# Kernel optimization log

Measured on AMD Instinct MI355X. Metric: run time of the kernel, lower is better.

Reference implementation:

```python
import jax, jax.numpy as jnp
import numpy as np
from jax import lax

T, B = 80, 32
ACT, CIN, HID, LSTM_H = 16, 4, 512, 256

def _conv(x, w, b, stride, pad):
    y = lax.conv_general_dilated(x, w, (stride, stride), [(pad, pad), (pad, pad)],
                                 dimension_numbers=('NCHW', 'OIHW', 'NCHW'))
    return y + b[None, :, None, None]

def setup_inputs() -> dict:
    key = jax.random.key(0)
    ks = jax.random.split(key, 20)
    s = 0.02
    return {
        'x': jax.random.uniform(ks[0], (T, B, CIN, 84, 84), dtype=jnp.float32),
        'last_action': jax.random.randint(ks[1], (T, B), 0, ACT),
        'reward': jax.random.normal(ks[2], (T, B), dtype=jnp.float32),
        'dones': jnp.zeros((T, B), dtype=bool),
        'hx': jax.random.normal(ks[3], (2, B, LSTM_H), dtype=jnp.float32) * s,
        'conv1_w': jax.random.normal(ks[4], (32, CIN, 8, 8), jnp.float32) * s,
        'conv1_b': jnp.zeros((32,), jnp.float32),
        'conv2_w': jax.random.normal(ks[5], (64, 32, 4, 4), jnp.float32) * s,
        'conv2_b': jnp.zeros((64,), jnp.float32),
        'conv3_w': jax.random.normal(ks[6], (64, 64, 3, 3), jnp.float32) * s,
        'conv3_b': jnp.zeros((64,), jnp.float32),
        'fc_w': jax.random.normal(ks[7], (HID, 3136), jnp.float32) * s,
        'fc_b': jnp.zeros((HID,), jnp.float32),
        'lstm_wih': jax.random.normal(ks[8], (4 * LSTM_H, HID + ACT + 1), jnp.float32) * s,
        'lstm_whh': jax.random.normal(ks[9], (4 * LSTM_H, LSTM_H), jnp.float32) * s,
        'lstm_bih': jnp.zeros((4 * LSTM_H,), jnp.float32),
        'lstm_bhh': jnp.zeros((4 * LSTM_H,), jnp.float32),
        'actor_w': jax.random.normal(ks[10], (ACT, LSTM_H), jnp.float32) * s,
        'actor_b': jnp.zeros((ACT,), jnp.float32),
        'critic_w': jax.random.normal(ks[11], (1, LSTM_H), jnp.float32) * s,
        'critic_b': jnp.zeros((1,), jnp.float32),
    }

def reference(x, last_action, reward, dones, hx,
              conv1_w, conv1_b, conv2_w, conv2_b, conv3_w, conv3_b,
              fc_w, fc_b, lstm_wih, lstm_whh, lstm_bih, lstm_bhh,
              actor_w, actor_b, critic_w, critic_b):
    seq_len, bs = x.shape[0], x.shape[1]
    xf = x.reshape(seq_len * bs, CIN, 84, 84)          # combine time & batch
    la = jax.nn.one_hot(last_action.reshape(-1), ACT, dtype=jnp.float32)
    rw = reward.reshape(-1, 1)

    lrelu = lambda v: jax.nn.leaky_relu(v, 0.01)
    h = lrelu(_conv(xf, conv1_w, conv1_b, 4, 1))       # [N,32,20,20]
    h = lrelu(_conv(h, conv2_w, conv2_b, 2, 0))        # [N,64,9,9]
    h = lrelu(_conv(h, conv3_w, conv3_b, 1, 0))        # [N,64,7,7]
    h = h.reshape(h.shape[0], -1)                      # [N,3136]
    h = lrelu(h @ fc_w.T + fc_b)                       # [N,512]
    h = jnp.concatenate([h, rw, la], axis=1)           # [N,529]
    h = h.reshape(seq_len, bs, -1)

    def step(carry, inp):
        xt, dt = inp                                   # [bs,529], [bs] bool
        carry = jnp.where(dt[None, :, None], 0.0, carry)
        hh, cc = carry[0], carry[1]
        gates = xt @ lstm_wih.T + lstm_bih + hh @ lstm_whh.T + lstm_bhh
        i, f, g, o = jnp.split(gates, 4, axis=1)
        cc = jax.nn.sigmoid(f) * cc + jax.nn.sigmoid(i) * jnp.tanh(g)
        hh = jax.nn.sigmoid(o) * jnp.tanh(cc)
        return jnp.stack([hh, cc], 0), hh

    _, hs = lax.scan(step, hx, (h, dones))             # hs: [T,bs,256]
    feat = hs.reshape(seq_len * bs, LSTM_H)

    logits = feat @ actor_w.T + actor_b                # [N,16]
    values = feat @ critic_w.T + critic_b              # [N,1]
    logits = jnp.where(jnp.isnan(logits), jnp.float32(1e-12), logits)
    return logits.reshape(seq_len, -1, bs), values.reshape(seq_len, bs)
```

## Files before the change

kernel.cpp:

```cpp
#include <hip/hip_runtime.h>
#include <math.h>

#define T_ 80
#define B_ 32
#define N_ 2560
#define LH_ 256

typedef __attribute__((ext_vector_type(8))) short short8;
typedef __attribute__((ext_vector_type(4))) float f32x4;
#define MFMA16(a, b, c) __builtin_amdgcn_mfma_f32_16x16x32_bf16((a), (b), (c), 0, 0, 0)

__device__ __forceinline__ float lrelu(float v) { return v > 0.f ? v : 0.01f * v; }
__device__ __forceinline__ short f2bf(float f) {
    unsigned u = __float_as_uint(f);
    return (short)((u + 0x7fffu + ((u >> 16) & 1u)) >> 16);
}

__global__ void pack_all_k(const float* __restrict__ c1w, const float* __restrict__ c2w,
                           const float* __restrict__ c3w, const float* __restrict__ fcw,
                           const float* __restrict__ wih,
                           short* __restrict__ wp1, short* __restrict__ wp2,
                           short* __restrict__ wp3, short* __restrict__ wfcP,
                           short* __restrict__ wihP, int* __restrict__ cnt) {
    int blk = blockIdx.x, tidx = threadIdx.x;
    if (blk < 6272) {
        int g = blk * 256 + tidx;
        int j = g / 3136, kp = g % 3136, p = kp >> 6, oc = kp & 63;
        wfcP[g] = f2bf(fcw[j * 3136 + oc * 49 + p]);
        return;
    }
    blk -= 6272;
    if (blk < 2048) {
        int g = blk * 256 + tidx;
        int r = g >> 9, k = g & 511;
        wihP[g] = f2bf(wih[r * 529 + k]);
        return;
    }
    blk -= 2048;
    if (blk < 32) {
        int g = blk * 256 + tidx;
        int ky = g >> 10, oc = (g >> 5) & 31, k = g & 31, kx = k >> 2, ci = k & 3;
        wp1[g] = f2bf(c1w[((oc * 4 + ci) * 8 + ky) * 8 + kx]);
        return;
    }
    blk -= 32;
    if (blk < 128) {
        int g = blk * 256 + tidx;
        int t = g >> 11, oc = (g >> 5) & 63, ci = g & 31, ky = t >> 2, kx = t & 3;
        wp2[g] = f2bf(c2w[((oc * 32 + ci) * 4 + ky) * 4 + kx]);
        return;
    }
    blk -= 128;
    if (blk < 144) {
        int g = blk * 256 + tidx;
        int tkc = g >> 11, oc = (g >> 5) & 63, c32 = g & 31;
        int t = tkc >> 1, kc = tkc & 1, ky = t / 3, kx = t % 3;
        wp3[g] = f2bf(c3w[((oc * 64 + kc * 32 + c32) * 3 + ky) * 3 + kx]);
        return;
    }
    cnt[tidx] = 0; cnt[256 + tidx] = 0;
}

#define C1_RS 344
__global__ __launch_bounds__(512) void conv1_mfma(
    const float* __restrict__ x, const short* __restrict__ wp1,
    const float* __restrict__ bias, short* __restrict__ h1) {
    __shared__ short xs[44 * C1_RS];
    __shared__ short ob[208 * 32];
    int blk = blockIdx.x, n = blk >> 1, h = blk & 1, tid = threadIdx.x;
    for (int i = tid; i < 44 * 84; i += 512) {
        int ry = i / 84, xi4 = i % 84;
        int ci = xi4 / 21, x4 = xi4 % 21;
        int iy = ry + h * 40 - 1;
        if (iy < 0 || iy > 83) continue;
        float4 v = *(const float4*)(x + (size_t)(n * 4 + ci) * 7056 + iy * 84 + x4 * 4);
        int base = ry * C1_RS + (x4 * 4 + 1) * 4 + ci;
        xs[base] = f2bf(v.x); xs[base + 4] = f2bf(v.y);
        xs[base + 8] = f2bf(v.z); xs[base + 12] = f2bf(v.w);
    }
    for (int i = tid; i < 44 * 4; i += 512)
        xs[(i >> 2) * C1_RS + (i & 3)] = 0;
    if (h == 0) for (int i = tid; i < C1_RS; i += 512) xs[i] = 0;
    __syncthreads();

    int lane = tid & 63, wid = tid >> 6;
    int lr = lane & 15, kq = lane >> 4;
    short8 bfr[8][2];
#pragma unroll
    for (int ky = 0; ky < 8; ++ky)
#pragma unroll
        for (int nt = 0; nt < 2; ++nt)
            bfr[ky][nt] = *(const short8*)&wp1[((ky * 32) + nt * 16 + lr) * 32 + kq * 8];
    float b0 = bias[lr], b1 = bias[16 + lr];

    for (int t = wid; t < 13; t += 8) {
        int p = t * 16 + lr; if (p > 199) p = 199;
        int oy = p / 20, ox = p % 20;
        f32x4 acc0 = {0.f, 0.f, 0.f, 0.f}, acc1 = {0.f, 0.f, 0.f, 0.f};
#pragma unroll
        for (int ky = 0; ky < 8; ++ky) {
            int ry = oy * 4 + ky;
            short8 af = *(const short8*)&xs[ry * C1_RS + ox * 16 + kq * 8];
            acc0 = MFMA16(af, bfr[ky][0], acc0);
            acc1 = MFMA16(af, bfr[ky][1], acc1);
        }
        int pm = t * 16 + kq * 4;
#pragma unroll
        for (int r = 0; r < 4; ++r) {
            ob[(pm + r) * 32 + lr]      = f2bf(lrelu(acc0[r] + b0));
            ob[(pm + r) * 32 + 16 + lr] = f2bf(lrelu(acc1[r] + b1));
        }
    }
    __syncthreads();
    uint4* dst = (uint4*)(h1 + (size_t)n * 12800 + h * 6400);
    for (int i = tid; i < 800; i += 512) dst[i] = ((uint4*)ob)[i];
}

__global__ __launch_bounds__(512) void conv23_mfma(
    const short* __restrict__ h1,
    const short* __restrict__ wp2, const float* __restrict__ b2v,
    const short* __restrict__ wp3, const float* __restrict__ b3v,
    short* __restrict__ h3) {
    __shared__ short in_s[400 * 40];
    __shared__ short ob2[96 * 72];
    int n = blockIdx.x, tid = threadIdx.x;
    const uint4* src = (const uint4*)(h1 + (size_t)n * 12800);
    for (int i = tid; i < 1600; i += 512)
        *(uint4*)&in_s[(i >> 2) * 40 + (i & 3) * 8] = src[i];
    __syncthreads();
    int lane = tid & 63, wid = tid >> 6;
    int nt = wid & 3, mh = wid >> 2;
    int lr = lane & 15, kq = lane >> 4;
    {
        short8 bfr[16];
#pragma unroll
        for (int t = 0; t < 16; ++t)
            bfr[t] = *(const short8*)&wp2[(t * 64 + nt * 16 + lr) * 32 + kq * 8];
        float bl = b2v[nt * 16 + lr];
        for (int mt = mh * 3; mt < mh * 3 + 3; ++mt) {
            int p = mt * 16 + lr; if (p > 80) p = 80;
            int oy = p / 9, ox = p % 9;
            f32x4 acc = {0.f, 0.f, 0.f, 0.f};
#pragma unroll
            for (int ky = 0; ky < 4; ++ky)
#pragma unroll
                for (int kx = 0; kx < 4; ++kx) {
                    int pix = (oy * 2 + ky) * 20 + ox * 2 + kx;
                    short8 af = *(const short8*)&in_s[pix * 40 + kq * 8];
                    acc = MFMA16(af, bfr[ky * 4 + kx], acc);
                }
            int pm = mt * 16 + kq * 4;
#pragma unroll
            for (int r = 0; r < 4; ++r)
                ob2[(pm + r) * 72 + nt * 16 + lr] = f2bf(lrelu(acc[r] + bl));
        }
    }
    __syncthreads();
    {
        short8 cfr[18];
#pragma unroll
        for (int t = 0; t < 18; ++t)
            cfr[t] = *(const short8*)&wp3[(t * 64 + nt * 16 + lr) * 32 + kq * 8];
        float bl3 = b3v[nt * 16 + lr];
        short* ob3 = in_s;
        for (int mt = mh * 2; mt < mh * 2 + 2; ++mt) {
            int p = mt * 16 + lr; if (p > 48) p = 48;
            int oy = p / 7, ox = p % 7;
            f32x4 acc = {0.f, 0.f, 0.f, 0.f};
#pragma unroll
            for (int ky = 0; ky < 3; ++ky)
#pragma unroll
                for (int kx = 0; kx < 3; ++kx) {
                    int pix = (oy + ky) * 9 + ox + kx;
#pragma unroll
                    for (int kc = 0; kc < 2; ++kc) {
                        short8 af = *(const short8*)&ob2[pix * 72 + kc * 32 + kq * 8];
                        acc = MFMA16(af, cfr[(ky * 3 + kx) * 2 + kc], acc);
                    }
                }
            int pm = mt * 16 + kq * 4;
#pragma unroll
            for (int r = 0; r < 4; ++r)
                ob3[(pm + r) * 64 + nt * 16 + lr] = f2bf(lrelu(acc[r] + bl3));
        }
    }
    __syncthreads();
    uint4* dst = (uint4*)(h3 + (size_t)n * 3136);
    for (int i = tid; i < 392; i += 512) dst[i] = ((uint4*)in_s)[i];
}

template <int OUT>
__global__ __launch_bounds__(256) void gemm_bf16(
    const short* __restrict__ A, const short* __restrict__ B,
    const float* __restrict__ bias, void* __restrict__ Cout,
    int M, int N, int K, int ldc,
    const float* __restrict__ reward = nullptr, const int* __restrict__ la = nullptr,
    const float* __restrict__ wih = nullptr, const float* __restrict__ bih = nullptr,
    const float* __restrict__ bhh = nullptr) {
    __shared__ short smem[20480];
    int m0 = blockIdx.y * 128, n0 = blockIdx.x * 128;
    int tid = threadIdx.x;
    int lane = tid & 63, wid = tid >> 6;
    int wr = wid >> 1, wc = wid & 1;
    int lr = lane & 15, kq = lane >> 4;
    f32x4 acc[4][4];
#pragma unroll
    for (int i = 0; i < 4; ++i)
#pragma unroll
        for (int j = 0; j < 4; ++j) acc[i][j] = (f32x4){0.f, 0.f, 0.f, 0.f};

    int nsteps = K >> 5;
#define STAGE(k0, buf)                                                          \
    {                                                                           \
        short* As = smem + (buf) * 5120;                                        \
        short* Bs = smem + 10240 + (buf) * 5120;                                \
        for (int i = tid; i < 512; i += 256) {                                  \
            int row = i >> 2, c4 = i & 3;                                       \
            *(uint4*)&As[row * 40 + c4 * 8] =                                   \
                *(const uint4*)&A[(size_t)(m0 + row) * K + (k0) + c4 * 8];      \
            *(uint4*)&Bs[row * 40 + c4 * 8] =                                   \
                *(const uint4*)&B[(size_t)(n0 + row) * K + (k0) + c4 * 8];      \
        }                                                                       \
    }
    STAGE(0, 0);
    __syncthreads();
    for (int ks = 0; ks < nsteps; ++ks) {
        int buf = ks & 1;
        if (ks + 1 < nsteps) STAGE((ks + 1) * 32, buf ^ 1);
        short* As = smem + buf * 5120;
        short* Bs = smem + 10240 + buf * 5120;
        short8 af[4], bfr[4];
#pragma unroll
        for (int i = 0; i < 4; ++i)
            af[i] = *(const short8*)&As[(wr * 64 + i * 16 + lr) * 40 + kq * 8];
#pragma unroll
        for (int j = 0; j < 4; ++j)
            bfr[j] = *(const short8*)&Bs[(wc * 64 + j * 16 + lr) * 40 + kq * 8];
#pragma unroll
        for (int i = 0; i < 4; ++i)
#pragma unroll
            for (int j = 0; j < 4; ++j)
                acc[i][j] = MFMA16(af[i], bfr[j], acc[i][j]);
        __syncthreads();
    }
#undef STAGE
    if (OUT == 2) {
        float* C = (float*)Cout;
#pragma unroll
        for (int i = 0; i < 4; ++i)
#pragma unroll
            for (int j = 0; j < 4; ++j) {
                int col = n0 + wc * 64 + j * 16 + lr;
                const float* wrow = wih + (size_t)col * 529;
                float base = bih[col] + bhh[col];
                float w512 = wrow[512];
#pragma unroll
                for (int r = 0; r < 4; ++r) {
                    int row = m0 + wr * 64 + i * 16 + kq * 4 + r;
                    C[(size_t)row * ldc + col] =
                        acc[i][j][r] + base + reward[row] * w512 + wrow[513 + la[row]];
                }
            }
    } else {
        short* ob = smem;
#pragma unroll
        for (int i = 0; i < 4; ++i)
#pragma unroll
            for (int j = 0; j < 4; ++j) {
                int col = wc * 64 + j * 16 + lr;
                float bl = bias[n0 + col];
#pragma unroll
                for (int r = 0; r < 4; ++r) {
                    int row = wr * 64 + i * 16 + kq * 4 + r;
                    ob[row * 128 + col] = f2bf(lrelu(acc[i][j][r] + bl));
                }
            }
        __syncthreads();
        short* C = (short*)Cout;
        for (int i = tid; i < 2048; i += 256) {
            int row = i >> 4, c16 = i & 15;
            *(uint4*)&C[(size_t)(m0 + row) * ldc + n0 + c16 * 8] =
                *(uint4*)&ob[row * 128 + c16 * 8];
        }
    }
}

__global__ __launch_bounds__(512) void lstm16_k(
    const float* __restrict__ gx,
    const float* __restrict__ whh,
    const unsigned char* __restrict__ dones,
    const float* __restrict__ hx,
    float* __restrict__ hs,
    float* __restrict__ hpub,
    int* __restrict__ cnt) {
    const int tid = threadIdx.x;
    const int grp  = blockIdx.x & 7;
    const int half = blockIdx.x >> 3;
    const int lane = tid & 63, w = tid >> 6;
    const int gt = w >> 1, s2 = w & 1;
    const int lr = lane & 15, kq = lane >> 4;

    __shared__ short hB[16 * 264];
    __shared__ float gate_s[4][128][4];

    short8 afr[4][8];
#pragma unroll
    for (int mi = 0; mi < 4; ++mi) {
        int row = gt * 256 + half * 128 + s2 * 64 + mi * 16 + lr;
        const float* wr = whh + (size_t)row * 256;
#pragma unroll
        for (int kt = 0; kt < 8; ++kt) {
            int k0 = kt * 32 + kq * 8;
            float4 a = *(const float4*)(wr + k0);
            float4 b = *(const float4*)(wr + k0 + 4);
            short8 f;
            f[0] = f2bf(a.x); f[1] = f2bf(a.y); f[2] = f2bf(a.z); f[3] = f2bf(a.w);
            f[4] = f2bf(b.x); f[5] = f2bf(b.y); f[6] = f2bf(b.z); f[7] = f2bf(b.w);
            afr[mi][kt] = f;
        }
    }
    {
        int* ap = (int*)afr;
#pragma unroll
        for (int i = 0; i < 128; ++i) asm volatile("" : "+v"(ap[i]));
    }

    for (int i = tid; i < 12 * 264; i += 512) hB[4 * 264 + i] = 0;

    const int u = tid >> 2, bt = tid & 3;
    const int b = grp * 4 + bt, gu = half * 128 + u;
    float cc = hx[(size_t)B_ * LH_ + b * LH_ + gu];
    __syncthreads();

    const int mycnt = (grp * 2 + half) * 32, peercnt = (grp * 2 + (half ^ 1)) * 32;

    for (int t = 1; t <= T_; ++t) {
        const int nb0 = (t - 1) * B_;
        float gxv[4];
#pragma unroll
        for (int g2 = 0; g2 < 4; ++g2)
            gxv[g2] = gx[(size_t)(nb0 + b) * 1024 + g2 * 256 + gu];

        if (t > 1) {
            if (tid == 0) {
                while (__hip_atomic_load(&cnt[peercnt], __ATOMIC_ACQUIRE,
                                         __HIP_MEMORY_SCOPE_AGENT) < t - 1)
                    __builtin_amdgcn_s_sleep(1);
            }
            __syncthreads();
        }
#pragma unroll
        for (int l = 0; l < 2; ++l) {
            int e = tid + l * 512;
            int bt2 = e >> 8, k = e & 255;
            int b2 = grp * 4 + bt2;
            float hv = (t == 1) ? hx[b2 * LH_ + k]
                                : hpub[((t - 1) & 1) * 8192 + b2 * 256 + k];
            if (dones[nb0 + b2]) hv = 0.f;
            hB[bt2 * 264 + k] = f2bf(hv);
        }
        __syncthreads();

        f32x4 acc[4] = {{0.f,0.f,0.f,0.f},{0.f,0.f,0.f,0.f},
                        {0.f,0.f,0.f,0.f},{0.f,0.f,0.f,0.f}};
#pragma unroll
        for (int kt = 0; kt < 8; ++kt) {
            short8 bfr = *(const short8*)&hB[lr * 264 + kt * 32 + kq * 8];
#pragma unroll
            for (int mi = 0; mi < 4; ++mi)
                acc[mi] = MFMA16(afr[mi][kt], bfr, acc[mi]);
        }
        if (lr < 4) {
#pragma unroll
            for (int mi = 0; mi < 4; ++mi)
#pragma unroll
                for (int r = 0; r < 4; ++r)
                    gate_s[gt][s2 * 64 + mi * 16 + kq * 4 + r][lr] = acc[mi][r];
        }
        __syncthreads();

        {
            bool dn = dones[nb0 + b] != 0;
            float gi = gate_s[0][u][bt] + gxv[0];
            float gf = gate_s[1][u][bt] + gxv[1];
            float gg = gate_s[2][u][bt] + gxv[2];
            float go = gate_s[3][u][bt] + gxv[3];
            float ccv = dn ? 0.f : cc;
            float si = 1.f / (1.f + expf(-gi));
            float sf = 1.f / (1.f + expf(-gf));
            float so = 1.f / (1.f + expf(-go));
            float c2 = sf * ccv + si * tanhf(gg);
            float h2 = so * tanhf(c2);
            cc = c2;
            hs[(size_t)(nb0 + b) * LH_ + gu] = h2;
            __hip_atomic_store(&hpub[(t & 1) * 8192 + b * 256 + gu], h2,
                               __ATOMIC_RELAXED, __HIP_MEMORY_SCOPE_AGENT);
        }
        __syncthreads();
        if (tid == 0)
            __hip_atomic_store(&cnt[mycnt], t, __ATOMIC_RELEASE,
                               __HIP_MEMORY_SCOPE_AGENT);
    }
}

__global__ void head_k(const float* __restrict__ hs,
                       const float* __restrict__ aw, const float* __restrict__ ab,
                       const float* __restrict__ cw, const float* __restrict__ cb,
                       float* __restrict__ out) {
    int gid = blockIdx.x * 256 + threadIdx.x;
    if (gid >= N_ * 17) return;
    int n = gid / 17, r = gid % 17;
    const float* f = hs + (size_t)n * 256;
    if (r < 16) {
        const float* w = aw + r * 256;
        float acc = ab[r];
        for (int k = 0; k < 256; ++k) acc = fmaf(f[k], w[k], acc);
        if (isnan(acc)) acc = 1e-12f;
        out[(size_t)n * 16 + r] = acc;
    } else {
        float acc = cb[0];
        for (int k = 0; k < 256; ++k) acc = fmaf(f[k], cw[k], acc);
        out[(size_t)N_ * 16 + n] = acc;
    }
}

extern "C" void kernel_launch(void* const* d_in, const int* in_sizes, int n_in,
                              void* d_out, int out_size, void* d_ws, size_t ws_size,
                              hipStream_t stream) {
    const float* x      = (const float*)d_in[0];
    const int* la       = (const int*)d_in[1];
    const float* reward = (const float*)d_in[2];
    const unsigned char* dones = (const unsigned char*)d_in[3];
    const float* hx     = (const float*)d_in[4];
    const float* c1w = (const float*)d_in[5];  const float* c1b = (const float*)d_in[6];
    const float* c2w = (const float*)d_in[7];  const float* c2b = (const float*)d_in[8];
    const float* c3w = (const float*)d_in[9];  const float* c3b = (const float*)d_in[10];
    const float* fcw = (const float*)d_in[11]; const float* fcb = (const float*)d_in[12];
    const float* wih = (const float*)d_in[13]; const float* whh = (const float*)d_in[14];
    const float* bih = (const float*)d_in[15]; const float* bhh = (const float*)d_in[16];
    const float* aw  = (const float*)d_in[17]; const float* ab  = (const float*)d_in[18];
    const float* cw  = (const float*)d_in[19]; const float* cb  = (const float*)d_in[20];

    char* wsb = (char*)d_ws;
    short* h1   = (short*)(wsb);
    short* h3   = (short*)(wsb + 92078080);
    short* hfc  = (short*)(wsb + 108134400);
    float* gx   = (float*)(wsb + 110755840);
    float* hs   = (float*)(wsb + 121241600);
    float* hpub = (float*)(wsb + 123863040);
    int*   cnt  = (int*)  (wsb + 123928576);
    short* wp1  = (short*)(wsb + 123932672);
    short* wp2  = (short*)(wsb + 123949056);
    short* wp3  = (short*)(wsb + 124014592);
    short* wfcP = (short*)(wsb + 124088320);
    short* wihP = (short*)(wsb + 127299584);

    pack_all_k<<<8625, 256, 0, stream>>>(c1w, c2w, c3w, fcw, wih,
                                         wp1, wp2, wp3, wfcP, wihP, cnt);

    conv1_mfma<<<5120, 512, 0, stream>>>(x, wp1, c1b, h1);
    conv23_mfma<<<2560, 512, 0, stream>>>(h1, wp2, c2b, wp3, c3b, h3);

    gemm_bf16<1><<<dim3(4, 20), 256, 0, stream>>>(h3, wfcP, fcb, hfc,
                                                  2560, 512, 3136, 512);
    gemm_bf16<2><<<dim3(8, 20), 256, 0, stream>>>(hfc, wihP, nullptr, gx,
                                                  2560, 1024, 512, 1024,
                                                  reward, la, wih, bih, bhh);

    lstm16_k<<<16, 512, 0, stream>>>(gx, whh, dones, hx, hs, hpub, cnt);
    head_k<<<170, 256, 0, stream>>>(hs, aw, ab, cw, cb, (float*)d_out);
}
```

Baseline: 538.2 us.

## Halve GEMM N-tile and exchange only peer half of LSTM hidden state in bf16

The bf16 GEMM tile shrinks from 128x128 to 128x64, which doubles the grid to 160/320 blocks so more CUs are busy on the 256-CU device. The LSTM kernel now writes its own half of the new hidden state straight into shared memory, with the done-mask and bf16 conversion applied. It publishes that half to global memory as bf16 and reads only the peer block's 128 values each step instead of all 256 floats. This shortens the per-step cross-block exchange on the serial recurrence, at the cost of lower MFMA reuse per GEMM block.

```diff
diff --git a/kernel.cpp b/kernel.cpp
--- a/kernel.cpp
+++ b/kernel.cpp
@@ -197,27 +197,30 @@
     const float* __restrict__ reward = nullptr, const int* __restrict__ la = nullptr,
     const float* __restrict__ wih = nullptr, const float* __restrict__ bih = nullptr,
     const float* __restrict__ bhh = nullptr) {
-    __shared__ short smem[20480];
-    int m0 = blockIdx.y * 128, n0 = blockIdx.x * 128;
+    __shared__ short smem[15360];
+    int m0 = blockIdx.y * 128, n0 = blockIdx.x * 64;
     int tid = threadIdx.x;
     int lane = tid & 63, wid = tid >> 6;
     int wr = wid >> 1, wc = wid & 1;
     int lr = lane & 15, kq = lane >> 4;
-    f32x4 acc[4][4];
+    f32x4 acc[4][2];
 #pragma unroll
     for (int i = 0; i < 4; ++i)
 #pragma unroll
-        for (int j = 0; j < 4; ++j) acc[i][j] = (f32x4){0.f, 0.f, 0.f, 0.f};
+        for (int j = 0; j < 2; ++j) acc[i][j] = (f32x4){0.f, 0.f, 0.f, 0.f};
 
     int nsteps = K >> 5;
 #define STAGE(k0, buf)                                                          \
     {                                                                           \
         short* As = smem + (buf) * 5120;                                        \
-        short* Bs = smem + 10240 + (buf) * 5120;                                \
+        short* Bs = smem + 10240 + (buf) * 2560;                                \
         for (int i = tid; i < 512; i += 256) {                                  \
             int row = i >> 2, c4 = i & 3;                                       \
             *(uint4*)&As[row * 40 + c4 * 8] =                                   \
                 *(const uint4*)&A[(size_t)(m0 + row) * K + (k0) + c4 * 8];      \
+        }                                                                       \
+        {                                                                       \
+            int row = tid >> 2, c4 = tid & 3;                                   \
             *(uint4*)&Bs[row * 40 + c4 * 8] =                                   \
                 *(const uint4*)&B[(size_t)(n0 + row) * K + (k0) + c4 * 8];      \
         }                                                                       \
@@ -228,18 +231,18 @@
         int buf = ks & 1;
         if (ks + 1 < nsteps) STAGE((ks + 1) * 32, buf ^ 1);
         short* As = smem + buf * 5120;
-        short* Bs = smem + 10240 + buf * 5120;
-        short8 af[4], bfr[4];
+        short* Bs = smem + 10240 + buf * 2560;
+        short8 af[4], bfr[2];
 #pragma unroll
         for (int i = 0; i < 4; ++i)
             af[i] = *(const short8*)&As[(wr * 64 + i * 16 + lr) * 40 + kq * 8];
 #pragma unroll
-        for (int j = 0; j < 4; ++j)
-            bfr[j] = *(const short8*)&Bs[(wc * 64 + j * 16 + lr) * 40 + kq * 8];
+        for (int j = 0; j < 2; ++j)
+            bfr[j] = *(const short8*)&Bs[(wc * 32 + j * 16 + lr) * 40 + kq * 8];
 #pragma unroll
         for (int i = 0; i < 4; ++i)
 #pragma unroll
-            for (int j = 0; j < 4; ++j)
+            for (int j = 0; j < 2; ++j)
                 acc[i][j] = MFMA16(af[i], bfr[j], acc[i][j]);
         __syncthreads();
     }
@@ -249,8 +252,8 @@
 #pragma unroll
         for (int i = 0; i < 4; ++i)
 #pragma unroll
-            for (int j = 0; j < 4; ++j) {
-                int col = n0 + wc * 64 + j * 16 + lr;
+            for (int j = 0; j < 2; ++j) {
+                int col = n0 + wc * 32 + j * 16 + lr;
                 const float* wrow = wih + (size_t)col * 529;
                 float base = bih[col] + bhh[col];
                 float w512 = wrow[512];
@@ -266,21 +269,21 @@
 #pragma unroll
         for (int i = 0; i < 4; ++i)
 #pragma unroll
-            for (int j = 0; j < 4; ++j) {
-                int col = wc * 64 + j * 16 + lr;
+            for (int j = 0; j < 2; ++j) {
+                int col = wc * 32 + j * 16 + lr;
                 float bl = bias[n0 + col];
 #pragma unroll
                 for (int r = 0; r < 4; ++r) {
                     int row = wr * 64 + i * 16 + kq * 4 + r;
-                    ob[row * 128 + col] = f2bf(lrelu(acc[i][j][r] + bl));
+                    ob[row * 64 + col] = f2bf(lrelu(acc[i][j][r] + bl));
                 }
             }
         __syncthreads();
         short* C = (short*)Cout;
-        for (int i = tid; i < 2048; i += 256) {
-            int row = i >> 4, c16 = i & 15;
-            *(uint4*)&C[(size_t)(m0 + row) * ldc + n0 + c16 * 8] =
-                *(uint4*)&ob[row * 128 + c16 * 8];
+        for (int i = tid; i < 1024; i += 256) {
+            int row = i >> 3, c8 = i & 7;
+            *(uint4*)&C[(size_t)(m0 + row) * ldc + n0 + c8 * 8] =
+                *(uint4*)&ob[row * 64 + c8 * 8];
         }
     }
 }
@@ -291,7 +294,7 @@
     const unsigned char* __restrict__ dones,
     const float* __restrict__ hx,
     float* __restrict__ hs,
-    float* __restrict__ hpub,
+    unsigned short* __restrict__ hpub,
     int* __restrict__ cnt) {
     const int tid = threadIdx.x;
     const int grp  = blockIdx.x & 7;
@@ -330,9 +333,20 @@
     const int u = tid >> 2, bt = tid & 3;
     const int b = grp * 4 + bt, gu = half * 128 + u;
     float cc = hx[(size_t)B_ * LH_ + b * LH_ + gu];
+
+#pragma unroll
+    for (int l = 0; l < 2; ++l) {
+        int e = tid + l * 512;
+        int bt2 = e >> 8, k = e & 255;
+        int b2 = grp * 4 + bt2;
+        float hv = hx[b2 * LH_ + k];
+        if (dones[b2]) hv = 0.f;
+        hB[bt2 * 264 + k] = f2bf(hv);
+    }
     __syncthreads();
 
     const int mycnt = (grp * 2 + half) * 32, peercnt = (grp * 2 + (half ^ 1)) * 32;
+    const int phalf = (half ^ 1) << 7;
 
     for (int t = 1; t <= T_; ++t) {
         const int nb0 = (t - 1) * B_;
@@ -348,16 +362,10 @@
                     __builtin_amdgcn_s_sleep(1);
             }
             __syncthreads();
-        }
-#pragma unroll
-        for (int l = 0; l < 2; ++l) {
-            int e = tid + l * 512;
-            int bt2 = e >> 8, k = e & 255;
-            int b2 = grp * 4 + bt2;
-            float hv = (t == 1) ? hx[b2 * LH_ + k]
-                                : hpub[((t - 1) & 1) * 8192 + b2 * 256 + k];
-            if (dones[nb0 + b2]) hv = 0.f;
-            hB[bt2 * 264 + k] = f2bf(hv);
+            int bt2 = tid >> 7, pu = tid & 127;
+            int b2 = grp * 4 + bt2, pgu = phalf + pu;
+            hB[bt2 * 264 + pgu] =
+                (short)hpub[((t - 1) & 1) * 8192 + b2 * 256 + pgu];
         }
         __syncthreads();
 
@@ -393,8 +401,11 @@
             float h2 = so * tanhf(c2);
             cc = c2;
             hs[(size_t)(nb0 + b) * LH_ + gu] = h2;
-            __hip_atomic_store(&hpub[(t & 1) * 8192 + b * 256 + gu], h2,
-                               __ATOMIC_RELAXED, __HIP_MEMORY_SCOPE_AGENT);
+            if (t < T_) {
+                short hm = f2bf(dones[t * B_ + b] ? 0.f : h2);
+                hB[bt * 264 + gu] = hm;
+                hpub[(t & 1) * 8192 + b * 256 + gu] = (unsigned short)hm;
+            }
         }
         __syncthreads();
         if (tid == 0)
@@ -447,7 +458,7 @@
     short* hfc  = (short*)(wsb + 108134400);
     float* gx   = (float*)(wsb + 110755840);
     float* hs   = (float*)(wsb + 121241600);
-    float* hpub = (float*)(wsb + 123863040);
+    unsigned short* hpub = (unsigned short*)(wsb + 123863040);
     int*   cnt  = (int*)  (wsb + 123928576);
     short* wp1  = (short*)(wsb + 123932672);
     short* wp2  = (short*)(wsb + 123949056);
@@ -461,11 +472,11 @@
     conv1_mfma<<<5120, 512, 0, stream>>>(x, wp1, c1b, h1);
     conv23_mfma<<<2560, 512, 0, stream>>>(h1, wp2, c2b, wp3, c3b, h3);
 
-    gemm_bf16<1><<<dim3(4, 20), 256, 0, stream>>>(h3, wfcP, fcb, hfc,
+    gemm_bf16<1><<<dim3(8, 20), 256, 0, stream>>>(h3, wfcP, fcb, hfc,
                                                   2560, 512, 3136, 512);
-    gemm_bf16<2><<<dim3(8, 20), 256, 0, stream>>>(hfc, wihP, nullptr, gx,
-                                                  2560, 1024, 512, 1024,
-                                                  reward, la, wih, bih, bhh);
+    gemm_bf16<2><<<dim3(16, 20), 256, 0, stream>>>(hfc, wihP, nullptr, gx,
+                                                   2560, 1024, 512, 1024,
+                                                   reward, la, wih, bih, bhh);
 
     lstm16_k<<<16, 512, 0, stream>>>(gx, whh, dones, hx, hs, hpub, cnt);
     head_k<<<170, 256, 0, stream>>>(hs, aw, ab, cw, cb, (float*)d_out);
```

Result: no change. 528.6 us (-1.8%).
